# Performance work log

Measured on AMD Instinct MI355X. Metric: run time of the kernel, lower is better.

Reference implementation:

```python
import jax, jax.numpy as jnp
import numpy as np

IN_FEATURES = 4096
OUT_FEATURES = 4096
BATCH = 8192
SPARSITY = 0.9


def setup_inputs() -> dict:
    key = jax.random.key(0)
    kx, kw, km = jax.random.split(key, 3)
    x = jax.random.normal(kx, (BATCH, IN_FEATURES), dtype=jnp.float32)
    weight = jax.random.normal(kw, (OUT_FEATURES, IN_FEATURES), dtype=jnp.float32)
    mask = jax.random.uniform(km, (OUT_FEATURES, IN_FEATURES)) > SPARSITY
    return {"x": x, "weight": weight, "mask": mask}


def reference(x, weight, mask):
    # CSR spMM of (weight*mask) with x^T, then transpose == x @ (weight*mask)^T
    w_sparse = weight * mask.astype(weight.dtype)  # [out, in]
    return jnp.einsum('bi,oi->bo', x, w_sparse)    # [batch, out]
```

## Files before the change

### kernel.cpp

```cpp
#include <hip/hip_runtime.h>
#include <hip/hip_bf16.h>
#include <stdint.h>

#define BATCH 8192
#define KDIM  4096
#define NDIM  4096

#define BM 256
#define BN 256
#define BK 64
#define NT (KDIM / BK)

typedef __bf16 bf16x8 __attribute__((ext_vector_type(8)));
typedef float  f32x4  __attribute__((ext_vector_type(4)));

__device__ inline float bf2f(uint32_t h) {
    union { uint32_t u; float f; } c; c.u = h << 16; return c.f;
}
__device__ inline uint32_t pk2(float a, float b) {
    union { __hip_bfloat16 h[2]; uint32_t u; } o;
    o.h[0] = __float2bfloat16(a); o.h[1] = __float2bfloat16(b);
    return o.u;
}

__global__ void detect_kernel(const uint32_t* __restrict__ x,
                              const uint32_t* __restrict__ w,
                              const uint32_t* __restrict__ m,
                              int* __restrict__ flags) {
    __shared__ int cx, cw, all01, allf32, anybf16;
    if (threadIdx.x == 0) { cx = 0; cw = 0; all01 = 1; allf32 = 1; anybf16 = 0; }
    __syncthreads();
    int lcx = 0, lcw = 0, la01 = 1, laf = 1, lab = 0;
    #pragma unroll
    for (int jj = 0; jj < 16; ++jj) {
        int i = jj * 256 + threadIdx.x;
        uint32_t vx = x[i], vw = w[i], vm = m[i];
        uint32_t ex = (vx >> 7) & 0xFFu; if (ex >= 0x70u && ex <= 0x86u) lcx++;
        uint32_t ew = (vw >> 7) & 0xFFu; if (ew >= 0x70u && ew <= 0x86u) lcw++;
        if (vm > 1u) la01 = 0;
        if (vm != 0u && vm != 0x3F800000u) laf = 0;
        if ((vm & 0xFFFFu) == 0x3F80u || (vm >> 16) == 0x3F80u) lab = 1;
    }
    atomicAdd(&cx, lcx); atomicAdd(&cw, lcw);
    if (!la01) atomicAnd(&all01, 0);
    if (!laf)  atomicAnd(&allf32, 0);
    if (lab)   atomicOr(&anybf16, 1);
    __syncthreads();
    if (threadIdx.x == 0) {
        flags[0] = (cx < 2048) ? 1 : 0;
        flags[1] = (cw < 2048) ? 1 : 0;
        int f;
        if (all01)        f = 0;
        else if (allf32)  f = 3;
        else if (anybf16) f = 2;
        else              f = 1;
        flags[2] = f;
    }
}

__global__ void xconv_kernel(const float4* __restrict__ xf,
                             uint2* __restrict__ xb2,
                             const int* __restrict__ flags) {
    if (flags[0] == 0) return;
    const int t = blockIdx.x * 256 + threadIdx.x;
    float4 a = xf[t];
    uint2 o; o.x = pk2(a.x, a.y); o.y = pk2(a.z, a.w);
    xb2[t] = o;
}

__global__ void wmask_kernel(const void* __restrict__ w,
                             const void* __restrict__ mask,
                             const int*  __restrict__ flags,
                             uint2* __restrict__ wm2) {
    const int fw = flags[1], fm = flags[2];
    const int t = blockIdx.x * 256 + threadIdx.x;
    float wv[4];
    if (fw) {
        float4 a = ((const float4*)w)[t];
        wv[0] = a.x; wv[1] = a.y; wv[2] = a.z; wv[3] = a.w;
    } else {
        uint2 wb = ((const uint2*)w)[t];
        wv[0] = bf2f(wb.x & 0xFFFFu); wv[1] = bf2f(wb.x >> 16);
        wv[2] = bf2f(wb.y & 0xFFFFu); wv[3] = bf2f(wb.y >> 16);
    }
    int kb[4];
    if (fm == 1) {
        uint32_t m1 = ((const uint32_t*)mask)[t];
        kb[0] = (m1 & 0xFFu) != 0u;         kb[1] = ((m1 >> 8) & 0xFFu) != 0u;
        kb[2] = ((m1 >> 16) & 0xFFu) != 0u; kb[3] = (m1 >> 24) != 0u;
    } else if (fm == 2) {
        uint2 m2 = ((const uint2*)mask)[t];
        kb[0] = (m2.x & 0xFFFFu) != 0u; kb[1] = (m2.x >> 16) != 0u;
        kb[2] = (m2.y & 0xFFFFu) != 0u; kb[3] = (m2.y >> 16) != 0u;
    } else {
        uint4 m4 = ((const uint4*)mask)[t];
        kb[0] = m4.x != 0u; kb[1] = m4.y != 0u; kb[2] = m4.z != 0u; kb[3] = m4.w != 0u;
    }
    uint2 o;
    o.x = pk2(kb[0] ? wv[0] : 0.0f, kb[1] ? wv[1] : 0.0f);
    o.y = pk2(kb[2] ? wv[2] : 0.0f, kb[3] ? wv[3] : 0.0f);
    wm2[t] = o;
}

__global__ __launch_bounds__(512, 2)
void gemm_bt_kernel(const uint16_t* __restrict__ Araw,
                    const uint16_t* __restrict__ Aconv,
                    const uint16_t* __restrict__ B,
                    void* __restrict__ Cout,
                    const int* __restrict__ flags) {
    __shared__ char smem[131072];

    const int fx = flags[0];
    const uint16_t* A = fx ? Aconv : Araw;

    const int bid = blockIdx.x;
    const int wid = (bid & 7) * 64 + (bid >> 3);
    const int m0  = (wid >> 4) * BM;
    const int n0  = (wid & 15) * BN;

    const int tid  = threadIdx.x;
    const int lane = tid & 63;
    const int wave = tid >> 6;
    const int wm_  = wave >> 2;
    const int wn_  = wave & 3;

    const int tL = tid >> 3;
    const uint32_t srcSlot = (uint32_t)(((tid & 7) ^ (tL & 7)) * 16);
    const size_t K2 = (size_t)KDIM * 2;
    const char* aS[2][2]; const char* bS[2][2];
    #pragma unroll
    for (int h = 0; h < 2; ++h)
        #pragma unroll
        for (int c = 0; c < 2; ++c) {
            const int r = h * 128 + tL + c * 64;
            aS[h][c] = (const char*)A + (size_t)(m0 + r) * K2 + srcSlot;
            bS[h][c] = (const char*)B + (size_t)(n0 + r) * K2 + srcSlot;
        }
    const uint32_t wdst = (uint32_t)(wave * 1024);

#define ISSUE_A(P, H, V) do {                                                   \
    const size_t kb_ = (size_t)(V) * 128;                                       \
    __builtin_amdgcn_global_load_lds(                                           \
        (__attribute__((address_space(1))) void*)(aS[H][0] + kb_),              \
        (__attribute__((address_space(3))) void*)(smem + (P)*65536 + (H)*16384 + wdst), 16, 0, 0); \
    __builtin_amdgcn_global_load_lds(                                           \
        (__attribute__((address_space(1))) void*)(aS[H][1] + kb_),              \
        (__attribute__((address_space(3))) void*)(smem + (P)*65536 + (H)*16384 + 8192 + wdst), 16, 0, 0); \
} while (0)

#define ISSUE_B(P, H, V) do {                                                   \
    const size_t kb_ = (size_t)(V) * 128;                                       \
    __builtin_amdgcn_global_load_lds(                                           \
        (__attribute__((address_space(1))) void*)(bS[H][0] + kb_),              \
        (__attribute__((address_space(3))) void*)(smem + (P)*65536 + 32768 + (H)*16384 + wdst), 16, 0, 0); \
    __builtin_amdgcn_global_load_lds(                                           \
        (__attribute__((address_space(1))) void*)(bS[H][1] + kb_),              \
        (__attribute__((address_space(3))) void*)(smem + (P)*65536 + 32768 + (H)*16384 + 8192 + wdst), 16, 0, 0); \
} while (0)

    const int fr = lane & 15;
    const int lq = lane >> 4;
    const uint32_t swz0 = (uint32_t)(((0 + lq) ^ (fr & 7)) * 16);
    const uint32_t swz1 = (uint32_t)(((4 + lq) ^ (fr & 7)) * 16);
    const uint32_t aRow = (uint32_t)((wm_ * 64 + fr) * 128);
    const uint32_t bRow = (uint32_t)((wn_ * 32 + fr) * 128);

    bf16x8 a[4][2], b[4][2];
    f32x4 acc[8][4] = {};

#define RD_A(P, H) do {                                                         \
    _Pragma("unroll")                                                           \
    for (int mi = 0; mi < 4; ++mi) {                                            \
        a[mi][0] = *(const bf16x8*)(smem + (P)*65536 + (H)*16384 + mi*2048 + aRow + swz0); \
        a[mi][1] = *(const bf16x8*)(smem + (P)*65536 + (H)*16384 + mi*2048 + aRow + swz1); \
    }                                                                           \
} while (0)

#define RD_B(P, H) do {                                                         \
    _Pragma("unroll")                                                           \
    for (int ni = 0; ni < 2; ++ni) {                                            \
        b[(H)*2+ni][0] = *(const bf16x8*)(smem + (P)*65536 + 32768 + (H)*16384 + ni*2048 + bRow + swz0); \
        b[(H)*2+ni][1] = *(const bf16x8*)(smem + (P)*65536 + 32768 + (H)*16384 + ni*2048 + bRow + swz1); \
    }                                                                           \
} while (0)

#define MFMA_Q(M0, N0) do {                                                     \
    _Pragma("unroll")                                                           \
    for (int mi = 0; mi < 4; ++mi)                                              \
        _Pragma("unroll")                                                       \
        for (int ni = 0; ni < 2; ++ni) {                                        \
            acc[(M0)+mi][(N0)+ni] = __builtin_amdgcn_mfma_f32_16x16x32_bf16(    \
                a[mi][0], b[(N0)+ni][0], acc[(M0)+mi][(N0)+ni], 0, 0, 0);       \
            acc[(M0)+mi][(N0)+ni] = __builtin_amdgcn_mfma_f32_16x16x32_bf16(    \
                a[mi][1], b[(N0)+ni][1], acc[(M0)+mi][(N0)+ni], 0, 0, 0);       \
        }                                                                       \
} while (0)

#define BAR() do { asm volatile("" ::: "memory");                               \
    __builtin_amdgcn_s_barrier();                                               \
    asm volatile("" ::: "memory"); } while (0)

#define TILE(P, V) do {                                                         \
                                \
    RD_A(P, 0); RD_B(P, 0); RD_B(P, 1);                                         \
    if ((V) + 1 < NT) ISSUE_A(1-(P), 1, (V)+1);                                 \
    __builtin_amdgcn_s_setprio(1);  MFMA_Q(0, 0);  __builtin_amdgcn_s_setprio(0); \
    BAR();                                                                      \
            \
    if ((V) + 1 < NT) ISSUE_B(1-(P), 1, (V)+1);                                 \
    __builtin_amdgcn_s_setprio(1);  MFMA_Q(0, 2);  __builtin_amdgcn_s_setprio(0); \
    RD_A(P, 1);                                                                 \
    BAR();                                                                      \
                                       \
    if ((V) + 2 < NT) ISSUE_A(P, 0, (V)+2);                                     \
    __builtin_amdgcn_s_setprio(1);  MFMA_Q(4, 0);  __builtin_amdgcn_s_setprio(0); \
    BAR();                                                                      \
                                          \
    if ((V) + 2 < NT) ISSUE_B(P, 0, (V)+2);                                     \
    __builtin_amdgcn_s_setprio(1);  MFMA_Q(4, 2);  __builtin_amdgcn_s_setprio(0); \
    if ((V) < NT - 2) { asm volatile("s_waitcnt vmcnt(4)" ::: "memory"); }      \
    else              { asm volatile("s_waitcnt vmcnt(0)" ::: "memory"); }      \
    BAR();                                                                      \
} while (0)

    ISSUE_A(0, 0, 0); ISSUE_B(0, 0, 0); ISSUE_B(0, 1, 0); ISSUE_A(0, 1, 0);
    asm volatile("s_waitcnt vmcnt(0)" ::: "memory");
    ISSUE_A(1, 0, 1); ISSUE_B(1, 0, 1);
    BAR();

    for (int it = 0; it < NT; it += 2) {
        TILE(0, it);
        TILE(1, it + 1);
    }

#undef TILE
#undef BAR
#undef MFMA_Q
#undef RD_B
#undef RD_A
#undef ISSUE_B
#undef ISSUE_A

    const int cn = lane & 15;
    const int rq = lane >> 4;
    if (fx) {
        float* C = (float*)Cout;
        #pragma unroll
        for (int mi = 0; mi < 8; ++mi)
            #pragma unroll
            for (int ni = 0; ni < 4; ++ni)
                #pragma unroll
                for (int r = 0; r < 4; ++r) {
                    const int gm = m0 + (mi >> 2) * 128 + wm_ * 64 + (mi & 3) * 16 + rq * 4 + r;
                    const int gn = n0 + (ni >> 1) * 128 + wn_ * 32 + (ni & 1) * 16 + cn;
                    C[(size_t)gm * NDIM + gn] = acc[mi][ni][r];
                }
    } else {
        __hip_bfloat16* C = (__hip_bfloat16*)Cout;
        #pragma unroll
        for (int mi = 0; mi < 8; ++mi)
            #pragma unroll
            for (int ni = 0; ni < 4; ++ni)
                #pragma unroll
                for (int r = 0; r < 4; ++r) {
                    const int gm = m0 + (mi >> 2) * 128 + wm_ * 64 + (mi & 3) * 16 + rq * 4 + r;
                    const int gn = n0 + (ni >> 1) * 128 + wn_ * 32 + (ni & 1) * 16 + cn;
                    C[(size_t)gm * NDIM + gn] = __float2bfloat16(acc[mi][ni][r]);
                }
    }
}

extern "C" void kernel_launch(void* const* d_in, const int* in_sizes, int n_in,
                              void* d_out, int out_size, void* d_ws, size_t ws_size,
                              hipStream_t stream) {
    const void* x    = d_in[0];
    const void* w    = d_in[1];
    const void* mask = d_in[2];

    int*      flags = (int*)d_ws;
    uint16_t* wm    = (uint16_t*)((char*)d_ws + 256);
    uint16_t* xb    = (uint16_t*)((char*)d_ws + 256 + (size_t)NDIM * KDIM * 2);

    detect_kernel<<<1, 256, 0, stream>>>((const uint32_t*)x, (const uint32_t*)w,
                                         (const uint32_t*)mask, flags);

    xconv_kernel<<<(BATCH * KDIM / 4) / 256, 256, 0, stream>>>(
        (const float4*)x, (uint2*)xb, flags);

    wmask_kernel<<<(NDIM * KDIM / 4) / 256, 256, 0, stream>>>(
        w, mask, flags, (uint2*)wm);

    gemm_bt_kernel<<<dim3((BATCH / BM) * (NDIM / BN)), 512, 0, stream>>>(
        (const uint16_t*)x, xb, wm, d_out, flags);
}
```

Measured before the change: 505.5 us.

## Restructure GEMM tile schedule with split fragment registers and cross-tile prefetch

Splits the A/B register fragments into separate halves (a0/a1, b0/b1) so LDS reads of the next half overlap the MFMAs on the current half. It also reorders the global-to-LDS issue sequence so the next tile's first A/B fragments are read during the last MFMA quadrant of the current tile. The intent is to hide LDS read latency and smooth the barrier-separated phases. The cost is more live registers, which risks spills or lower occupancy, and a changed vmcnt wait schedule that must stay correct.

```diff
diff --git a/kernel.cpp b/kernel.cpp
--- a/kernel.cpp
+++ b/kernel.cpp
@@ -165,34 +165,50 @@
     const uint32_t aRow = (uint32_t)((wm_ * 64 + fr) * 128);
     const uint32_t bRow = (uint32_t)((wn_ * 32 + fr) * 128);
 
-    bf16x8 a[4][2], b[4][2];
+    bf16x8 a0[4][2], a1[4][2], b0[2][2], b1[2][2];
     f32x4 acc[8][4] = {};
 
-#define RD_A(P, H) do {                                                         \
+#define RD_A0(P) do {                                                           \
     _Pragma("unroll")                                                           \
     for (int mi = 0; mi < 4; ++mi) {                                            \
-        a[mi][0] = *(const bf16x8*)(smem + (P)*65536 + (H)*16384 + mi*2048 + aRow + swz0); \
-        a[mi][1] = *(const bf16x8*)(smem + (P)*65536 + (H)*16384 + mi*2048 + aRow + swz1); \
+        a0[mi][0] = *(const bf16x8*)(smem + (P)*65536 + mi*2048 + aRow + swz0); \
+        a0[mi][1] = *(const bf16x8*)(smem + (P)*65536 + mi*2048 + aRow + swz1); \
     }                                                                           \
 } while (0)
 
-#define RD_B(P, H) do {                                                         \
+#define RD_A1(P) do {                                                           \
+    _Pragma("unroll")                                                           \
+    for (int mi = 0; mi < 4; ++mi) {                                            \
+        a1[mi][0] = *(const bf16x8*)(smem + (P)*65536 + 16384 + mi*2048 + aRow + swz0); \
+        a1[mi][1] = *(const bf16x8*)(smem + (P)*65536 + 16384 + mi*2048 + aRow + swz1); \
+    }                                                                           \
+} while (0)
+
+#define RD_B0(P) do {                                                           \
     _Pragma("unroll")                                                           \
     for (int ni = 0; ni < 2; ++ni) {                                            \
-        b[(H)*2+ni][0] = *(const bf16x8*)(smem + (P)*65536 + 32768 + (H)*16384 + ni*2048 + bRow + swz0); \
-        b[(H)*2+ni][1] = *(const bf16x8*)(smem + (P)*65536 + 32768 + (H)*16384 + ni*2048 + bRow + swz1); \
+        b0[ni][0] = *(const bf16x8*)(smem + (P)*65536 + 32768 + ni*2048 + bRow + swz0); \
+        b0[ni][1] = *(const bf16x8*)(smem + (P)*65536 + 32768 + ni*2048 + bRow + swz1); \
     }                                                                           \
 } while (0)
 
-#define MFMA_Q(M0, N0) do {                                                     \
+#define RD_B1(P) do {                                                           \
+    _Pragma("unroll")                                                           \
+    for (int ni = 0; ni < 2; ++ni) {                                            \
+        b1[ni][0] = *(const bf16x8*)(smem + (P)*65536 + 49152 + ni*2048 + bRow + swz0); \
+        b1[ni][1] = *(const bf16x8*)(smem + (P)*65536 + 49152 + ni*2048 + bRow + swz1); \
+    }                                                                           \
+} while (0)
+
+#define MFMA_Q(M0, N0, AF, BF) do {                                             \
     _Pragma("unroll")                                                           \
     for (int mi = 0; mi < 4; ++mi)                                              \
         _Pragma("unroll")                                                       \
         for (int ni = 0; ni < 2; ++ni) {                                        \
             acc[(M0)+mi][(N0)+ni] = __builtin_amdgcn_mfma_f32_16x16x32_bf16(    \
-                a[mi][0], b[(N0)+ni][0], acc[(M0)+mi][(N0)+ni], 0, 0, 0);       \
+                AF[mi][0], BF[ni][0], acc[(M0)+mi][(N0)+ni], 0, 0, 0);          \
             acc[(M0)+mi][(N0)+ni] = __builtin_amdgcn_mfma_f32_16x16x32_bf16(    \
-                a[mi][1], b[(N0)+ni][1], acc[(M0)+mi][(N0)+ni], 0, 0, 0);       \
+                AF[mi][1], BF[ni][1], acc[(M0)+mi][(N0)+ni], 0, 0, 0);          \
         }                                                                       \
 } while (0)
 
@@ -201,32 +217,39 @@
     asm volatile("" ::: "memory"); } while (0)
 
 #define TILE(P, V) do {                                                         \
-                                \
-    RD_A(P, 0); RD_B(P, 0); RD_B(P, 1);                                         \
-    if ((V) + 1 < NT) ISSUE_A(1-(P), 1, (V)+1);                                 \
-    __builtin_amdgcn_s_setprio(1);  MFMA_Q(0, 0);  __builtin_amdgcn_s_setprio(0); \
+                \
+    if ((V) + 1 < NT) ISSUE_B(1-(P), 0, (V)+1);                                 \
+    RD_B1(P);                                                                   \
+    __builtin_amdgcn_s_setprio(1);  MFMA_Q(0, 0, a0, b0);                       \
+    __builtin_amdgcn_s_setprio(0);                                              \
     BAR();                                                                      \
-            \
+                                        \
     if ((V) + 1 < NT) ISSUE_B(1-(P), 1, (V)+1);                                 \
-    __builtin_amdgcn_s_setprio(1);  MFMA_Q(0, 2);  __builtin_amdgcn_s_setprio(0); \
-    RD_A(P, 1);                                                                 \
+    RD_A1(P);                                                                   \
+    __builtin_amdgcn_s_setprio(1);  MFMA_Q(0, 2, a0, b1);                       \
+    __builtin_amdgcn_s_setprio(0);                                              \
     BAR();                                                                      \
-                                       \
+                          \
     if ((V) + 2 < NT) ISSUE_A(P, 0, (V)+2);                                     \
-    __builtin_amdgcn_s_setprio(1);  MFMA_Q(4, 0);  __builtin_amdgcn_s_setprio(0); \
-    BAR();                                                                      \
-                                          \
-    if ((V) + 2 < NT) ISSUE_B(P, 0, (V)+2);                                     \
-    __builtin_amdgcn_s_setprio(1);  MFMA_Q(4, 2);  __builtin_amdgcn_s_setprio(0); \
-    if ((V) < NT - 2) { asm volatile("s_waitcnt vmcnt(4)" ::: "memory"); }      \
+    __builtin_amdgcn_s_setprio(1);  MFMA_Q(4, 0, a1, b0);                       \
+    __builtin_amdgcn_s_setprio(0);                                              \
+    if ((V) + 2 < NT) { asm volatile("s_waitcnt vmcnt(2)" ::: "memory"); }      \
     else              { asm volatile("s_waitcnt vmcnt(0)" ::: "memory"); }      \
     BAR();                                                                      \
-} while (0)
-
-    ISSUE_A(0, 0, 0); ISSUE_B(0, 0, 0); ISSUE_B(0, 1, 0); ISSUE_A(0, 1, 0);
+              \
+    if ((V) + 2 < NT) ISSUE_A(P, 1, (V)+2);                                     \
+    if ((V) + 1 < NT) { RD_A0(1-(P)); RD_B0(1-(P)); }                           \
+    __builtin_amdgcn_s_setprio(1);  MFMA_Q(4, 2, a1, b1);                       \
+    __builtin_amdgcn_s_setprio(0);                                              \
+    BAR();                                                                      \
+} while (0)
+
+    ISSUE_A(0, 0, 0); ISSUE_A(0, 1, 0); ISSUE_B(0, 0, 0); ISSUE_B(0, 1, 0);
     asm volatile("s_waitcnt vmcnt(0)" ::: "memory");
-    ISSUE_A(1, 0, 1); ISSUE_B(1, 0, 1);
     BAR();
+    ISSUE_A(1, 0, 1);
+    ISSUE_A(1, 1, 1);
+    RD_A0(0); RD_B0(0);
 
     for (int it = 0; it < NT; it += 2) {
         TILE(0, it);
@@ -236,8 +259,10 @@
 #undef TILE
 #undef BAR
 #undef MFMA_Q
-#undef RD_B
-#undef RD_A
+#undef RD_B1
+#undef RD_B0
+#undef RD_A1
+#undef RD_A0
 #undef ISSUE_B
 #undef ISSUE_A
 
```

After: 863.6 us. 1.71x slower.

## Halve K-tile to 32 and simplify pipeline to single-barrier double buffer

Applied to the files above, without the earlier changes.

Reduces BK from 64 to 32, halving LDS use to 64KB, and replaces the four-phase, two-tiles-ahead load schedule with a plain double buffer. Each tile issues all global-to-LDS loads for the next tile, reads all fragments, runs all MFMAs, then waits on vmcnt(0) and takes one barrier. The warp-to-output mapping and the LDS swizzle change to fit the new layout. This cuts barrier count and code complexity, but it doubles the number of iterations and drops the deeper prefetch and the interleaving of MFMAs with loads. That can expose more memory latency per tile.

```diff
diff --git a/kernel.cpp b/kernel.cpp
--- a/kernel.cpp
+++ b/kernel.cpp
@@ -8,7 +8,7 @@
 
 #define BM 256
 #define BN 256
-#define BK 64
+#define BK 32
 #define NT (KDIM / BK)
 
 typedef __bf16 bf16x8 __attribute__((ext_vector_type(8)));
@@ -108,7 +108,7 @@
                     const uint16_t* __restrict__ B,
                     void* __restrict__ Cout,
                     const int* __restrict__ flags) {
-    __shared__ char smem[131072];
+    __shared__ char smem[65536];
 
     const int fx = flags[0];
     const uint16_t* A = fx ? Aconv : Araw;
@@ -124,76 +124,58 @@
     const int wm_  = wave >> 2;
     const int wn_  = wave & 3;
 
-    const int tL = tid >> 3;
-    const uint32_t srcSlot = (uint32_t)(((tid & 7) ^ (tL & 7)) * 16);
+    const int tRow  = tid >> 2;
+    const uint32_t tSlot = (uint32_t)(((tid & 3) ^ ((tid >> 3) & 3)) * 16);
     const size_t K2 = (size_t)KDIM * 2;
-    const char* aS[2][2]; const char* bS[2][2];
+    const char* aSrc[2]; const char* bSrc[2];
     #pragma unroll
-    for (int h = 0; h < 2; ++h)
-        #pragma unroll
-        for (int c = 0; c < 2; ++c) {
-            const int r = h * 128 + tL + c * 64;
-            aS[h][c] = (const char*)A + (size_t)(m0 + r) * K2 + srcSlot;
-            bS[h][c] = (const char*)B + (size_t)(n0 + r) * K2 + srcSlot;
-        }
+    for (int c = 0; c < 2; ++c) {
+        aSrc[c] = (const char*)A + (size_t)(m0 + c * 128 + tRow) * K2 + tSlot;
+        bSrc[c] = (const char*)B + (size_t)(n0 + c * 128 + tRow) * K2 + tSlot;
+    }
     const uint32_t wdst = (uint32_t)(wave * 1024);
 
-#define ISSUE_A(P, H, V) do {                                                   \
-    const size_t kb_ = (size_t)(V) * 128;                                       \
-    __builtin_amdgcn_global_load_lds(                                           \
-        (__attribute__((address_space(1))) void*)(aS[H][0] + kb_),              \
-        (__attribute__((address_space(3))) void*)(smem + (P)*65536 + (H)*16384 + wdst), 16, 0, 0); \
-    __builtin_amdgcn_global_load_lds(                                           \
-        (__attribute__((address_space(1))) void*)(aS[H][1] + kb_),              \
-        (__attribute__((address_space(3))) void*)(smem + (P)*65536 + (H)*16384 + 8192 + wdst), 16, 0, 0); \
-} while (0)
-
-#define ISSUE_B(P, H, V) do {                                                   \
-    const size_t kb_ = (size_t)(V) * 128;                                       \
-    __builtin_amdgcn_global_load_lds(                                           \
-        (__attribute__((address_space(1))) void*)(bS[H][0] + kb_),              \
-        (__attribute__((address_space(3))) void*)(smem + (P)*65536 + 32768 + (H)*16384 + wdst), 16, 0, 0); \
-    __builtin_amdgcn_global_load_lds(                                           \
-        (__attribute__((address_space(1))) void*)(bS[H][1] + kb_),              \
-        (__attribute__((address_space(3))) void*)(smem + (P)*65536 + 32768 + (H)*16384 + 8192 + wdst), 16, 0, 0); \
+#define ISSUE(P, V) do {                                                        \
+    const size_t kb_ = (size_t)(V) * 64;         \
+    __builtin_amdgcn_global_load_lds(                                           \
+        (__attribute__((address_space(1))) void*)(aSrc[0] + kb_),               \
+        (__attribute__((address_space(3))) void*)(smem + (P)*32768 + wdst), 16, 0, 0); \
+    __builtin_amdgcn_global_load_lds(                                           \
+        (__attribute__((address_space(1))) void*)(aSrc[1] + kb_),               \
+        (__attribute__((address_space(3))) void*)(smem + (P)*32768 + 8192 + wdst), 16, 0, 0); \
+    __builtin_amdgcn_global_load_lds(                                           \
+        (__attribute__((address_space(1))) void*)(bSrc[0] + kb_),               \
+        (__attribute__((address_space(3))) void*)(smem + (P)*32768 + 16384 + wdst), 16, 0, 0); \
+    __builtin_amdgcn_global_load_lds(                                           \
+        (__attribute__((address_space(1))) void*)(bSrc[1] + kb_),               \
+        (__attribute__((address_space(3))) void*)(smem + (P)*32768 + 24576 + wdst), 16, 0, 0); \
 } while (0)
 
     const int fr = lane & 15;
     const int lq = lane >> 4;
-    const uint32_t swz0 = (uint32_t)(((0 + lq) ^ (fr & 7)) * 16);
-    const uint32_t swz1 = (uint32_t)(((4 + lq) ^ (fr & 7)) * 16);
-    const uint32_t aRow = (uint32_t)((wm_ * 64 + fr) * 128);
-    const uint32_t bRow = (uint32_t)((wn_ * 32 + fr) * 128);
-
-    bf16x8 a[4][2], b[4][2];
+    const uint32_t swz = (uint32_t)((lq ^ ((fr >> 1) & 3)) * 16);
+    const uint32_t aRd = (uint32_t)((wm_ * 128 + fr) * 64) + swz;
+    const uint32_t bRd = 16384u + (uint32_t)((wn_ * 64 + fr) * 64) + swz;
+
+    bf16x8 a[8], b[4];
     f32x4 acc[8][4] = {};
 
-#define RD_A(P, H) do {                                                         \
+#define RD(P) do {                                                              \
     _Pragma("unroll")                                                           \
-    for (int mi = 0; mi < 4; ++mi) {                                            \
-        a[mi][0] = *(const bf16x8*)(smem + (P)*65536 + (H)*16384 + mi*2048 + aRow + swz0); \
-        a[mi][1] = *(const bf16x8*)(smem + (P)*65536 + (H)*16384 + mi*2048 + aRow + swz1); \
-    }                                                                           \
-} while (0)
-
-#define RD_B(P, H) do {                                                         \
+    for (int mi = 0; mi < 8; ++mi)                                              \
+        a[mi] = *(const bf16x8*)(smem + (P)*32768 + mi*1024 + aRd);             \
     _Pragma("unroll")                                                           \
-    for (int ni = 0; ni < 2; ++ni) {                                            \
-        b[(H)*2+ni][0] = *(const bf16x8*)(smem + (P)*65536 + 32768 + (H)*16384 + ni*2048 + bRow + swz0); \
-        b[(H)*2+ni][1] = *(const bf16x8*)(smem + (P)*65536 + 32768 + (H)*16384 + ni*2048 + bRow + swz1); \
-    }                                                                           \
-} while (0)
-
-#define MFMA_Q(M0, N0) do {                                                     \
+    for (int ni = 0; ni < 4; ++ni)                                              \
+        b[ni] = *(const bf16x8*)(smem + (P)*32768 + ni*1024 + bRd);             \
+} while (0)
+
+#define MFMA_ALL() do {                                                         \
     _Pragma("unroll")                                                           \
-    for (int mi = 0; mi < 4; ++mi)                                              \
+    for (int mi = 0; mi < 8; ++mi)                                              \
         _Pragma("unroll")                                                       \
-        for (int ni = 0; ni < 2; ++ni) {                                        \
-            acc[(M0)+mi][(N0)+ni] = __builtin_amdgcn_mfma_f32_16x16x32_bf16(    \
-                a[mi][0], b[(N0)+ni][0], acc[(M0)+mi][(N0)+ni], 0, 0, 0);       \
-            acc[(M0)+mi][(N0)+ni] = __builtin_amdgcn_mfma_f32_16x16x32_bf16(    \
-                a[mi][1], b[(N0)+ni][1], acc[(M0)+mi][(N0)+ni], 0, 0, 0);       \
-        }                                                                       \
+        for (int ni = 0; ni < 4; ++ni)                                          \
+            acc[mi][ni] = __builtin_amdgcn_mfma_f32_16x16x32_bf16(              \
+                a[mi], b[ni], acc[mi][ni], 0, 0, 0);                            \
 } while (0)
 
 #define BAR() do { asm volatile("" ::: "memory");                               \
@@ -201,31 +183,15 @@
     asm volatile("" ::: "memory"); } while (0)
 
 #define TILE(P, V) do {                                                         \
-                                \
-    RD_A(P, 0); RD_B(P, 0); RD_B(P, 1);                                         \
-    if ((V) + 1 < NT) ISSUE_A(1-(P), 1, (V)+1);                                 \
-    __builtin_amdgcn_s_setprio(1);  MFMA_Q(0, 0);  __builtin_amdgcn_s_setprio(0); \
+    if ((V) + 1 < NT) ISSUE(1-(P), (V)+1);                                      \
+    RD(P);                                                                      \
+    __builtin_amdgcn_s_setprio(1);  MFMA_ALL();  __builtin_amdgcn_s_setprio(0); \
+    asm volatile("s_waitcnt vmcnt(0)" ::: "memory");                            \
     BAR();                                                                      \
-            \
-    if ((V) + 1 < NT) ISSUE_B(1-(P), 1, (V)+1);                                 \
-    __builtin_amdgcn_s_setprio(1);  MFMA_Q(0, 2);  __builtin_amdgcn_s_setprio(0); \
-    RD_A(P, 1);                                                                 \
-    BAR();                                                                      \
-                                       \
-    if ((V) + 2 < NT) ISSUE_A(P, 0, (V)+2);                                     \
-    __builtin_amdgcn_s_setprio(1);  MFMA_Q(4, 0);  __builtin_amdgcn_s_setprio(0); \
-    BAR();                                                                      \
-                                          \
-    if ((V) + 2 < NT) ISSUE_B(P, 0, (V)+2);                                     \
-    __builtin_amdgcn_s_setprio(1);  MFMA_Q(4, 2);  __builtin_amdgcn_s_setprio(0); \
-    if ((V) < NT - 2) { asm volatile("s_waitcnt vmcnt(4)" ::: "memory"); }      \
-    else              { asm volatile("s_waitcnt vmcnt(0)" ::: "memory"); }      \
-    BAR();                                                                      \
-} while (0)
-
-    ISSUE_A(0, 0, 0); ISSUE_B(0, 0, 0); ISSUE_B(0, 1, 0); ISSUE_A(0, 1, 0);
+} while (0)
+
+    ISSUE(0, 0);
     asm volatile("s_waitcnt vmcnt(0)" ::: "memory");
-    ISSUE_A(1, 0, 1); ISSUE_B(1, 0, 1);
     BAR();
 
     for (int it = 0; it < NT; it += 2) {
@@ -235,11 +201,9 @@
 
 #undef TILE
 #undef BAR
-#undef MFMA_Q
-#undef RD_B
-#undef RD_A
-#undef ISSUE_B
-#undef ISSUE_A
+#undef MFMA_ALL
+#undef RD
+#undef ISSUE
 
     const int cn = lane & 15;
     const int rq = lane >> 4;
@@ -251,8 +215,8 @@
             for (int ni = 0; ni < 4; ++ni)
                 #pragma unroll
                 for (int r = 0; r < 4; ++r) {
-                    const int gm = m0 + (mi >> 2) * 128 + wm_ * 64 + (mi & 3) * 16 + rq * 4 + r;
-                    const int gn = n0 + (ni >> 1) * 128 + wn_ * 32 + (ni & 1) * 16 + cn;
+                    const int gm = m0 + wm_ * 128 + mi * 16 + rq * 4 + r;
+                    const int gn = n0 + wn_ * 64 + ni * 16 + cn;
                     C[(size_t)gm * NDIM + gn] = acc[mi][ni][r];
                 }
     } else {
@@ -263,8 +227,8 @@
             for (int ni = 0; ni < 4; ++ni)
                 #pragma unroll
                 for (int r = 0; r < 4; ++r) {
-                    const int gm = m0 + (mi >> 2) * 128 + wm_ * 64 + (mi & 3) * 16 + rq * 4 + r;
-                    const int gn = n0 + (ni >> 1) * 128 + wn_ * 32 + (ni & 1) * 16 + cn;
+                    const int gm = m0 + wm_ * 128 + mi * 16 + rq * 4 + r;
+                    const int gn = n0 + wn_ * 64 + ni * 16 + cn;
                     C[(size_t)gm * NDIM + gn] = __float2bfloat16(acc[mi][ni][r]);
                 }
     }
```

Measured after the change: 564.7 us. +11.7%, slower.
